# Kernel optimization log

Hardware: AMD Instinct MI355X
Metric: run time of the kernel (lower is better)

## Reference

```python
import jax, jax.numpy as jnp
import numpy as np

N, F, H, C, E = 100000, 64, 128, 10, 1600000
BN_EPS = 1e-5


def setup_inputs() -> dict:
    key = jax.random.key(0)
    ks = jax.random.split(key, 16)
    s = 0.05
    return {
        "x": jax.random.normal(ks[0], (N, F), dtype=jnp.float32),
        "edge_index": jax.random.randint(ks[1], (2, E), 0, N, dtype=jnp.int64),
        # conv1 MLP: Linear(F,H), ReLU, Linear(H,H)
        "w1a": jax.random.normal(ks[2], (F, H), dtype=jnp.float32) * s,
        "b1a": jnp.zeros((H,), jnp.float32),
        "w1b": jax.random.normal(ks[3], (H, H), dtype=jnp.float32) * s,
        "b1b": jnp.zeros((H,), jnp.float32),
        # conv2 MLP: Linear(H,H), ReLU, Linear(H,H)
        "w2a": jax.random.normal(ks[4], (H, H), dtype=jnp.float32) * s,
        "b2a": jnp.zeros((H,), jnp.float32),
        "w2b": jax.random.normal(ks[5], (H, H), dtype=jnp.float32) * s,
        "b2b": jnp.zeros((H,), jnp.float32),
        # BatchNorm affine params
        "bn1_g": jnp.ones((H,), jnp.float32),
        "bn1_b": jnp.zeros((H,), jnp.float32),
        "bn2_g": jnp.ones((H,), jnp.float32),
        "bn2_b": jnp.zeros((H,), jnp.float32),
        # classifier MLP: Linear(H,H), ReLU, (Dropout=identity), Linear(H,C)
        "mw1": jax.random.normal(ks[6], (H, H), dtype=jnp.float32) * s,
        "mb1": jnp.zeros((H,), jnp.float32),
        "mw2": jax.random.normal(ks[7], (H, C), dtype=jnp.float32) * s,
        "mb2": jnp.zeros((C,), jnp.float32),
    }


def _gin_conv(x, src, dst, wa, ba, wb, bb):
    # GINConv, eps=0: mlp( sum_{j in N(i)} x_j + x_i )
    agg = jax.ops.segment_sum(x[src], dst, num_segments=N) + x
    h = jax.nn.relu(agg @ wa + ba)
    return h @ wb + bb


def _batchnorm(h, g, b):
    mean = jnp.mean(h, axis=0)
    var = jnp.var(h, axis=0)  # biased, matches torch BN training normalization
    return (h - mean) * jax.lax.rsqrt(var + BN_EPS) * g + b


def reference(x, edge_index, w1a, b1a, w1b, b1b, w2a, b2a, w2b, b2b,
              bn1_g, bn1_b, bn2_g, bn2_b, mw1, mb1, mw2, mb2):
    src, dst = edge_index[0], edge_index[1]
    h = _gin_conv(x, src, dst, w1a, b1a, w1b, b1b)
    h = jax.nn.relu(_batchnorm(h, bn1_g, bn1_b))
    h = _gin_conv(h, src, dst, w2a, b2a, w2b, b2b)
    latent = jax.nn.relu(_batchnorm(h, bn2_g, bn2_b))
    # classifier (dropout = identity at inference)
    m = jax.nn.relu(latent @ mw1 + mb1)
    class_out = m @ mw2 + mb2
    return latent, class_out
```

## Files before the change

kernel.cpp:

```cpp
#include <hip/hip_runtime.h>
#include <cstdint>


#define NN 100000
#define FF 64
#define HH 128
#define CC 10
#define EE 1600000
#define BN_EPS 1e-5f
#define MBLK 128
#define NBLK_LIN ((NN + MBLK - 1) / MBLK)
#define BSHIFT 7
#define NBUCK ((NN + 127) / 128)
#define CHUNK 16384
#define NB_CH ((EE + CHUNK - 1) / CHUNK)
#define NB_CVT 3125
#define TW (8192 + 4 * 16384 + 2048)
#define TWB ((TW + 255) / 256)
#define LDSE 3072

typedef __attribute__((ext_vector_type(8))) short bf16x8;
typedef __attribute__((ext_vector_type(4))) float f32x4;

__device__ inline unsigned short f2bf(float f) {
    unsigned int u = __float_as_uint(f);
    unsigned int r = (u + 0x7fffu + ((u >> 16) & 1u)) >> 16;
    return (unsigned short)r;
}
__device__ inline float b2f(unsigned short h) {
    return __uint_as_float(((unsigned int)h) << 16);
}
__device__ inline unsigned int pack2(float a, float b) {
    return (unsigned int)f2bf(a) | ((unsigned int)f2bf(b) << 16);
}
__device__ inline int detect_i64(const unsigned int* e) {
    return (e[1] | e[3] | e[5] | e[7]) == 0u;
}
__device__ inline int edge_dst(const void* eiv, int f, int e) {
    return f ? (int)((const long long*)eiv)[EE + e] : ((const int*)eiv)[EE + e];
}
__device__ inline int edge_src(const void* eiv, int f, int e) {
    return f ? (int)((const long long*)eiv)[e] : ((const int*)eiv)[e];
}

__global__ __launch_bounds__(256) void cvtprep_kernel(
    const float* __restrict__ x, unsigned short* __restrict__ xb,
    const float* __restrict__ w1a, const float* __restrict__ w1b,
    const float* __restrict__ w2a, const float* __restrict__ w2b,
    const float* __restrict__ mw1, const float* __restrict__ mw2,
    unsigned short* __restrict__ wt1a, unsigned short* __restrict__ wt1b,
    unsigned short* __restrict__ wt2a, unsigned short* __restrict__ wt2b,
    unsigned short* __restrict__ wtm1, unsigned short* __restrict__ wtm2,
    float* __restrict__ stats, const void* __restrict__ eiv,
    int* __restrict__ chunkhist) {
    __shared__ int hist[NBUCK];
    const int tid = threadIdx.x;
    const int b = blockIdx.x;
    if (b == 0)
        for (int i = tid; i < 512; i += 256) stats[i] = 0.f;
    if (b < NB_CVT) {
        int i = b * 256 + tid;
        float4 a = ((const float4*)x)[i * 2];
        float4 c = ((const float4*)x)[i * 2 + 1];
        uint4 o;
        o.x = pack2(a.x, a.y); o.y = pack2(a.z, a.w);
        o.z = pack2(c.x, c.y); o.w = pack2(c.z, c.w);
        ((uint4*)xb)[i] = o;
        return;
    }
    if (b < NB_CVT + TWB) {
        int idx = (b - NB_CVT) * 256 + tid;
        if (idx < 8192) {
            int k = idx >> 7, n = idx & 127;
            wt1a[n * 64 + k] = f2bf(w1a[idx]);
        } else if (idx < 8192 + 16384) {
            int t = idx - 8192; int k = t >> 7, n = t & 127;
            wt1b[n * 128 + k] = f2bf(w1b[t]);
        } else if (idx < 8192 + 2 * 16384) {
            int t = idx - (8192 + 16384); int k = t >> 7, n = t & 127;
            wt2a[n * 128 + k] = f2bf(w2a[t]);
        } else if (idx < 8192 + 3 * 16384) {
            int t = idx - (8192 + 2 * 16384); int k = t >> 7, n = t & 127;
            wt2b[n * 128 + k] = f2bf(w2b[t]);
        } else if (idx < 8192 + 4 * 16384) {
            int t = idx - (8192 + 3 * 16384); int k = t >> 7, n = t & 127;
            wtm1[n * 128 + k] = f2bf(mw1[t]);
        } else if (idx < TW) {
            int t = idx - (8192 + 4 * 16384); int n = t & 15, k = t >> 4;
            wtm2[n * 128 + k] = (n < CC) ? f2bf(mw2[k * CC + n]) : (unsigned short)0;
        }
        return;
    }
    const int ch = b - NB_CVT - TWB;
    const int f = detect_i64((const unsigned int*)eiv);
    for (int i = tid; i < NBUCK; i += 256) hist[i] = 0;
    __syncthreads();
    int beg = ch * CHUNK, end = min(beg + CHUNK, EE);
    for (int e = beg + tid; e < end; e += 256)
        atomicAdd(&hist[edge_dst(eiv, f, e) >> BSHIFT], 1);
    __syncthreads();
    for (int i = tid; i < NBUCK; i += 256) chunkhist[ch * NBUCK + i] = hist[i];
}

__global__ __launch_bounds__(128) void chunkscan_kernel(int* __restrict__ chunkhist,
                                                        int* __restrict__ gbcount) {
    __shared__ int s[128];
    const int b = blockIdx.x, tid = threadIdx.x;
    int v = (tid < NB_CH) ? chunkhist[tid * NBUCK + b] : 0;
    s[tid] = v;
    __syncthreads();
    for (int off = 1; off < 128; off <<= 1) {
        int t = (tid >= off) ? s[tid - off] : 0;
        __syncthreads();
        s[tid] += t;
        __syncthreads();
    }
    if (tid < NB_CH) chunkhist[tid * NBUCK + b] = s[tid] - v;
    if (tid == 127) gbcount[b] = s[127];
}

__global__ __launch_bounds__(1024) void bscan_kernel(const int* __restrict__ gbcount,
                                                     int* __restrict__ gbstart,
                                                     int* __restrict__ rowstart) {
    __shared__ int s[1024];
    const int tid = threadIdx.x;
    int v = (tid < NBUCK) ? gbcount[tid] : 0;
    s[tid] = v;
    __syncthreads();
    for (int off = 1; off < 1024; off <<= 1) {
        int t = (tid >= off) ? s[tid - off] : 0;
        __syncthreads();
        s[tid] += t;
        __syncthreads();
    }
    if (tid < NBUCK) gbstart[tid] = s[tid] - v;
    if (tid == 0) { gbstart[NBUCK] = EE; rowstart[NN] = EE; }
}

__global__ __launch_bounds__(256) void p2_bin_kernel(const void* __restrict__ eiv,
                                                     const int* __restrict__ gbstart,
                                                     const int* __restrict__ relbase,
                                                     unsigned int* __restrict__ packed) {
    __shared__ int hist[NBUCK];
    __shared__ int basep[NBUCK];
    const int tid = threadIdx.x;
    const int ch = blockIdx.x;
    const int f = detect_i64((const unsigned int*)eiv);
    for (int i = tid; i < NBUCK; i += 256) {
        hist[i] = 0;
        basep[i] = gbstart[i] + relbase[ch * NBUCK + i];
    }
    __syncthreads();
    int beg = ch * CHUNK, end = min(beg + CHUNK, EE);
    for (int e = beg + tid; e < end; e += 256) {
        int s = edge_src(eiv, f, e);
        int d = edge_dst(eiv, f, e);
        int b = d >> BSHIFT;
        int r = atomicAdd(&hist[b], 1);
        packed[basep[b] + r] = (unsigned int)s | ((unsigned int)(d & 127) << 17);
    }
}

__global__ __launch_bounds__(256) void p3g1_kernel(const unsigned int* __restrict__ packed,
                                                   const int* __restrict__ gbstart,
                                                   const unsigned short* __restrict__ xb,
                                                   int* __restrict__ rowstart,
                                                   int* __restrict__ eidx,
                                                   unsigned short* __restrict__ agg1) {
    __shared__ int hist[128];
    __shared__ int excl[128];
    __shared__ int sc[128];
    __shared__ int lidx[LDSE];
    const int tid = threadIdx.x;
    const int b = blockIdx.x;
    const int bstart = gbstart[b], bend = gbstart[b + 1];
    const int cnt = bend - bstart;
    if (tid < 128) hist[tid] = 0;
    __syncthreads();
    for (int e = bstart + tid; e < bend; e += 256)
        atomicAdd(&hist[packed[e] >> 17], 1);
    __syncthreads();
    int v = (tid < 128) ? hist[tid] : 0;
    if (tid < 128) sc[tid] = v;
    __syncthreads();
    for (int off = 1; off < 128; off <<= 1) {
        int t = (tid < 128 && tid >= off) ? sc[tid - off] : 0;
        __syncthreads();
        if (tid < 128) sc[tid] += t;
        __syncthreads();
    }
    if (tid < 128) {
        excl[tid] = sc[tid] - v;
        hist[tid] = 0;
        int node = b * 128 + tid;
        if (node < NN) rowstart[node] = bstart + sc[tid] - v;
    }
    __syncthreads();
    const bool inl = (cnt <= LDSE);
    for (int e = bstart + tid; e < bend; e += 256) {
        unsigned int p = packed[e];
        int dl = p >> 17;
        int r = atomicAdd(&hist[dl], 1);
        int pos = excl[dl] + r;
        int sv = (int)(p & 0x1FFFFu);
        eidx[bstart + pos] = sv;
        if (inl) lidx[pos] = sv;
    }
    __syncthreads();
    const int* ep = inl ? (const int*)lidx : (eidx + bstart);
    const int g = tid >> 3, l8 = tid & 7, c = l8 * 8;
    for (int r4 = 0; r4 < 4; r4++) {
        int nl = r4 * 32 + g;
        int node = b * 128 + nl;
        if (node >= NN) continue;
        float acc[8];
        uint4 sv4 = *(const uint4*)(xb + (size_t)node * FF + c);
        {
            const unsigned int* wv = (const unsigned int*)&sv4;
#pragma unroll
            for (int p = 0; p < 4; p++) {
                acc[p * 2] = b2f((unsigned short)(wv[p] & 0xffff));
                acc[p * 2 + 1] = b2f((unsigned short)(wv[p] >> 16));
            }
        }
        auto addv = [&](uint4 u) {
            const unsigned int* wv = (const unsigned int*)&u;
#pragma unroll
            for (int p = 0; p < 4; p++) {
                acc[p * 2] += b2f((unsigned short)(wv[p] & 0xffff));
                acc[p * 2 + 1] += b2f((unsigned short)(wv[p] >> 16));
            }
        };
        int beg2 = excl[nl], cend = beg2 + hist[nl];
        int j = beg2;
        for (; j + 3 < cend; j += 4) {
            int i0 = ep[j], i1 = ep[j + 1], i2 = ep[j + 2], i3 = ep[j + 3];
            uint4 v0 = *(const uint4*)(xb + (size_t)i0 * FF + c);
            uint4 v1 = *(const uint4*)(xb + (size_t)i1 * FF + c);
            uint4 v2 = *(const uint4*)(xb + (size_t)i2 * FF + c);
            uint4 v3 = *(const uint4*)(xb + (size_t)i3 * FF + c);
            addv(v0); addv(v1); addv(v2); addv(v3);
        }
        for (; j < cend; j++)
            addv(*(const uint4*)(xb + (size_t)ep[j] * FF + c));
        uint4 o;
        o.x = pack2(acc[0], acc[1]); o.y = pack2(acc[2], acc[3]);
        o.z = pack2(acc[4], acc[5]); o.w = pack2(acc[6], acc[7]);
        *(uint4*)(agg1 + (size_t)node * FF + c) = o;
    }
}

__global__ __launch_bounds__(256) void gather2_kernel(const unsigned short* __restrict__ h,
                                                      const int* __restrict__ rowstart,
                                                      const int* __restrict__ eidx,
                                                      const float* __restrict__ statsum,
                                                      const float* __restrict__ statsq,
                                                      const float* __restrict__ bng,
                                                      const float* __restrict__ bnb,
                                                      unsigned short* __restrict__ agg2) {
    int node = blockIdx.x * 8 + (threadIdx.x >> 5);
    const int l32 = threadIdx.x & 31;
    const int c = l32 * 4;
    if (node >= NN) return;
    float scl[4], off[4];
#pragma unroll
    for (int k = 0; k < 4; k++) {
        float m = statsum[c + k] * (1.0f / NN);
        float vv = statsq[c + k] * (1.0f / NN) - m * m;
        scl[k] = bng[c + k] * rsqrtf(vv + BN_EPS);
        off[k] = bnb[c + k] - m * scl[k];
    }
    float acc[4] = {0.f, 0.f, 0.f, 0.f};
    auto addv = [&](uint2 u) {
        acc[0] += fmaxf(fmaf(b2f((unsigned short)(u.x & 0xffff)), scl[0], off[0]), 0.f);
        acc[1] += fmaxf(fmaf(b2f((unsigned short)(u.x >> 16)), scl[1], off[1]), 0.f);
        acc[2] += fmaxf(fmaf(b2f((unsigned short)(u.y & 0xffff)), scl[2], off[2]), 0.f);
        acc[3] += fmaxf(fmaf(b2f((unsigned short)(u.y >> 16)), scl[3], off[3]), 0.f);
    };
    addv(*(const uint2*)(h + (size_t)node * HH + c));
    int beg = rowstart[node], end = rowstart[node + 1];
    int j = beg;
    for (; j + 3 < end; j += 4) {
        int i0 = eidx[j], i1 = eidx[j + 1], i2 = eidx[j + 2], i3 = eidx[j + 3];
        uint2 v0 = *(const uint2*)(h + (size_t)i0 * HH + c);
        uint2 v1 = *(const uint2*)(h + (size_t)i1 * HH + c);
        uint2 v2 = *(const uint2*)(h + (size_t)i2 * HH + c);
        uint2 v3 = *(const uint2*)(h + (size_t)i3 * HH + c);
        addv(v0); addv(v1); addv(v2); addv(v3);
    }
    for (; j < end; j++)
        addv(*(const uint2*)(h + (size_t)eidx[j] * HH + c));
    uint2 o;
    o.x = pack2(acc[0], acc[1]);
    o.y = pack2(acc[2], acc[3]);
    *(uint2*)(agg2 + (size_t)node * HH + c) = o;
}

template <int KIN>
__global__ __launch_bounds__(256) void mlp_kernel(const unsigned short* __restrict__ in,
                                                  const unsigned short* __restrict__ wTa,
                                                  const float* __restrict__ ba,
                                                  const unsigned short* __restrict__ wTb,
                                                  const float* __restrict__ bb,
                                                  unsigned short* __restrict__ out,
                                                  float* __restrict__ bnsum,
                                                  float* __restrict__ bnsq) {
    constexpr int KLDA = KIN + 8;
    constexpr int CH = KIN / 8;
    __shared__ __attribute__((aligned(16))) unsigned short sA[MBLK * 136];
    __shared__ __attribute__((aligned(16))) unsigned short sW[128 * 136];
    __shared__ float sSt[256];
    __shared__ float sB[256];

    const int tid = threadIdx.x;
    const int wave = tid >> 6, lane = tid & 63;
    const int quad = lane >> 4, l16 = lane & 15;
    const long long row0 = (long long)blockIdx.x * MBLK;

    sSt[tid] = 0.f;
    if (tid < 128) sB[tid] = ba[tid];
    else sB[tid] = bb[tid - 128];

    for (int i = tid; i < 128 * CH; i += 256)
        *(uint4*)(sW + (i / CH) * KLDA + (i % CH) * 8) = ((const uint4*)wTa)[i];
    for (int i = tid; i < MBLK * CH; i += 256) {
        int r = i / CH, c = i % CH;
        uint4 v = {0u, 0u, 0u, 0u};
        if (row0 + r < NN) v = *(const uint4*)(in + (row0 + r) * KIN + c * 8);
        *(uint4*)(sA + r * KLDA + c * 8) = v;
    }
    __syncthreads();

    f32x4 acc1[2][8];
#pragma unroll
    for (int t = 0; t < 2; t++)
#pragma unroll
        for (int n = 0; n < 8; n++) acc1[t][n] = 0.f;
#pragma unroll
    for (int ks = 0; ks < KIN / 32; ks++) {
        bf16x8 a0 = *(const bf16x8*)(sA + (wave * 32 + l16) * KLDA + ks * 32 + quad * 8);
        bf16x8 a1 = *(const bf16x8*)(sA + (wave * 32 + 16 + l16) * KLDA + ks * 32 + quad * 8);
#pragma unroll
        for (int nt = 0; nt < 8; nt++) {
            bf16x8 b = *(const bf16x8*)(sW + (nt * 16 + l16) * KLDA + ks * 32 + quad * 8);
            acc1[0][nt] = __builtin_amdgcn_mfma_f32_16x16x32_bf16(a0, b, acc1[0][nt], 0, 0, 0);
            acc1[1][nt] = __builtin_amdgcn_mfma_f32_16x16x32_bf16(a1, b, acc1[1][nt], 0, 0, 0);
        }
    }
    __syncthreads();

#pragma unroll
    for (int nt = 0; nt < 8; nt++) {
        const int col = nt * 16 + l16;
        const float bcol = sB[col];
#pragma unroll
        for (int t = 0; t < 2; t++)
#pragma unroll
            for (int r = 0; r < 4; r++) {
                int rl = wave * 32 + t * 16 + quad * 4 + r;
                sA[rl * 136 + col] = f2bf(fmaxf(acc1[t][nt][r] + bcol, 0.f));
            }
    }
    for (int i = tid; i < 128 * 16; i += 256)
        *(uint4*)(sW + (i >> 4) * 136 + (i & 15) * 8) = ((const uint4*)wTb)[i];
    __syncthreads();

    f32x4 acc2[2][8];
#pragma unroll
    for (int t = 0; t < 2; t++)
#pragma unroll
        for (int n = 0; n < 8; n++) acc2[t][n] = 0.f;
#pragma unroll
    for (int ks = 0; ks < 4; ks++) {
        bf16x8 a0 = *(const bf16x8*)(sA + (wave * 32 + l16) * 136 + ks * 32 + quad * 8);
        bf16x8 a1 = *(const bf16x8*)(sA + (wave * 32 + 16 + l16) * 136 + ks * 32 + quad * 8);
#pragma unroll
        for (int nt = 0; nt < 8; nt++) {
            bf16x8 b = *(const bf16x8*)(sW + (nt * 16 + l16) * 136 + ks * 32 + quad * 8);
            acc2[0][nt] = __builtin_amdgcn_mfma_f32_16x16x32_bf16(a0, b, acc2[0][nt], 0, 0, 0);
            acc2[1][nt] = __builtin_amdgcn_mfma_f32_16x16x32_bf16(a1, b, acc2[1][nt], 0, 0, 0);
        }
    }
    __syncthreads();

#pragma unroll
    for (int nt = 0; nt < 8; nt++) {
        const int col = nt * 16 + l16;
        const float bcol = sB[128 + col];
        float ls = 0.f, lq = 0.f;
#pragma unroll
        for (int t = 0; t < 2; t++)
#pragma unroll
            for (int r = 0; r < 4; r++) {
                int rl = wave * 32 + t * 16 + quad * 4 + r;
                float v = acc2[t][nt][r] + bcol;
                if (row0 + rl < NN) { ls += v; lq += v * v; }
                sA[rl * 136 + col] = f2bf(v);
            }
        ls += __shfl_down(ls, 32); ls += __shfl_down(ls, 16);
        lq += __shfl_down(lq, 32); lq += __shfl_down(lq, 16);
        if (lane < 16) { atomicAdd(&sSt[col], ls); atomicAdd(&sSt[128 + col], lq); }
    }
    __syncthreads();

    for (int i = tid; i < MBLK * 16; i += 256) {
        int r = i >> 4, c = i & 15;
        if (row0 + r < NN)
            *(uint4*)(out + (row0 + r) * 128 + c * 8) = *(const uint4*)(sA + r * 136 + c * 8);
    }
    if (tid < 128) atomicAdd(&bnsum[tid], sSt[tid]);
    else atomicAdd(&bnsq[tid - 128], sSt[tid]);
}

__global__ __launch_bounds__(256) void final_kernel(const unsigned short* __restrict__ h2,
                                                    const float* __restrict__ statsum,
                                                    const float* __restrict__ statsq,
                                                    const float* __restrict__ bng,
                                                    const float* __restrict__ bnb,
                                                    const unsigned short* __restrict__ wTm1,
                                                    const float* __restrict__ mb1,
                                                    const unsigned short* __restrict__ wTm2,
                                                    const float* __restrict__ mb2,
                                                    float* __restrict__ latent,
                                                    float* __restrict__ cls) {
    __shared__ __attribute__((aligned(16))) unsigned short sA[MBLK * 136];
    __shared__ __attribute__((aligned(16))) unsigned short sW[128 * 136];
    __shared__ float sBN[256];
    __shared__ float sB1[128];

    const int tid = threadIdx.x;
    const int wave = tid >> 6, lane = tid & 63;
    const int quad = lane >> 4, l16 = lane & 15;
    const long long row0 = (long long)blockIdx.x * MBLK;

    if (tid < 128) {
        float mean = statsum[tid] * (1.0f / NN);
        float var = statsq[tid] * (1.0f / NN) - mean * mean;
        float sc = bng[tid] * rsqrtf(var + BN_EPS);
        sBN[tid] = sc;
        sBN[128 + tid] = bnb[tid] - mean * sc;
        sB1[tid] = mb1[tid];
    }
    for (int i = tid; i < 128 * 16; i += 256)
        *(uint4*)(sW + (i >> 4) * 136 + (i & 15) * 8) = ((const uint4*)wTm1)[i];
    __syncthreads();

    for (int i = tid; i < MBLK * 16; i += 256) {
        int r = i >> 4, c = i & 15;
        bool live = (row0 + r < NN);
        uint4 hv = {0u, 0u, 0u, 0u};
        if (live) hv = *(const uint4*)(h2 + (row0 + r) * 128 + c * 8);
        const unsigned int* wv = (const unsigned int*)&hv;
        float vs[8];
#pragma unroll
        for (int p = 0; p < 4; p++) {
            int cc = c * 8 + p * 2;
            vs[p * 2]     = fmaxf(fmaf(b2f((unsigned short)(wv[p] & 0xffff)), sBN[cc], sBN[128 + cc]), 0.f);
            vs[p * 2 + 1] = fmaxf(fmaf(b2f((unsigned short)(wv[p] >> 16)), sBN[cc + 1], sBN[129 + cc]), 0.f);
        }
        if (live) {
            float4 f0 = {vs[0], vs[1], vs[2], vs[3]};
            float4 f1 = {vs[4], vs[5], vs[6], vs[7]};
            float* lp = latent + (row0 + r) * 128 + c * 8;
            *(float4*)lp = f0;
            *(float4*)(lp + 4) = f1;
        }
        uint4 o;
        o.x = pack2(vs[0], vs[1]); o.y = pack2(vs[2], vs[3]);
        o.z = pack2(vs[4], vs[5]); o.w = pack2(vs[6], vs[7]);
        *(uint4*)(sA + r * 136 + c * 8) = o;
    }
    __syncthreads();

    f32x4 acc1[2][8];
#pragma unroll
    for (int t = 0; t < 2; t++)
#pragma unroll
        for (int n = 0; n < 8; n++) acc1[t][n] = 0.f;
#pragma unroll
    for (int ks = 0; ks < 4; ks++) {
        bf16x8 av0 = *(const bf16x8*)(sA + (wave * 32 + l16) * 136 + ks * 32 + quad * 8);
        bf16x8 av1 = *(const bf16x8*)(sA + (wave * 32 + 16 + l16) * 136 + ks * 32 + quad * 8);
#pragma unroll
        for (int nt = 0; nt < 8; nt++) {
            bf16x8 b = *(const bf16x8*)(sW + (nt * 16 + l16) * 136 + ks * 32 + quad * 8);
            acc1[0][nt] = __builtin_amdgcn_mfma_f32_16x16x32_bf16(av0, b, acc1[0][nt], 0, 0, 0);
            acc1[1][nt] = __builtin_amdgcn_mfma_f32_16x16x32_bf16(av1, b, acc1[1][nt], 0, 0, 0);
        }
    }
    __syncthreads();

#pragma unroll
    for (int nt = 0; nt < 8; nt++) {
        const int col = nt * 16 + l16;
        const float bcol = sB1[col];
#pragma unroll
        for (int t = 0; t < 2; t++)
#pragma unroll
            for (int r = 0; r < 4; r++) {
                int rl = wave * 32 + t * 16 + quad * 4 + r;
                sA[rl * 136 + col] = f2bf(fmaxf(acc1[t][nt][r] + bcol, 0.f));
            }
    }
    if (tid < 256)
        *(uint4*)(sW + (tid >> 4) * 136 + (tid & 15) * 8) = ((const uint4*)wTm2)[tid];
    __syncthreads();

    f32x4 acc2[2];
    acc2[0] = 0.f; acc2[1] = 0.f;
#pragma unroll
    for (int ks = 0; ks < 4; ks++) {
        bf16x8 av0 = *(const bf16x8*)(sA + (wave * 32 + l16) * 136 + ks * 32 + quad * 8);
        bf16x8 av1 = *(const bf16x8*)(sA + (wave * 32 + 16 + l16) * 136 + ks * 32 + quad * 8);
        bf16x8 b = *(const bf16x8*)(sW + l16 * 136 + ks * 32 + quad * 8);
        acc2[0] = __builtin_amdgcn_mfma_f32_16x16x32_bf16(av0, b, acc2[0], 0, 0, 0);
        acc2[1] = __builtin_amdgcn_mfma_f32_16x16x32_bf16(av1, b, acc2[1], 0, 0, 0);
    }
    __syncthreads();

    float* sOf = (float*)sA;
    if (l16 < CC) {
        const float bc = mb2[l16];
#pragma unroll
        for (int t = 0; t < 2; t++)
#pragma unroll
            for (int r = 0; r < 4; r++) {
                int rl = wave * 32 + t * 16 + quad * 4 + r;
                sOf[rl * CC + l16] = acc2[t][r] + bc;
            }
    }
    __syncthreads();
    for (int i = tid; i < MBLK * CC; i += 256) {
        long long gi = row0 * CC + i;
        if (gi < (long long)NN * CC) cls[gi] = sOf[i];
    }
}

extern "C" void kernel_launch(void* const* d_in, const int* in_sizes, int n_in,
                              void* d_out, int out_size, void* d_ws, size_t ws_size,
                              hipStream_t stream) {
    const float* x   = (const float*)d_in[0];
    const void* ei   = d_in[1];
    const float* w1a = (const float*)d_in[2];
    const float* b1a = (const float*)d_in[3];
    const float* w1b = (const float*)d_in[4];
    const float* b1b = (const float*)d_in[5];
    const float* w2a = (const float*)d_in[6];
    const float* b2a = (const float*)d_in[7];
    const float* w2b = (const float*)d_in[8];
    const float* b2b = (const float*)d_in[9];
    const float* bn1g = (const float*)d_in[10];
    const float* bn1b = (const float*)d_in[11];
    const float* bn2g = (const float*)d_in[12];
    const float* bn2b = (const float*)d_in[13];
    const float* mw1 = (const float*)d_in[14];
    const float* mb1 = (const float*)d_in[15];
    const float* mw2 = (const float*)d_in[16];
    const float* mb2 = (const float*)d_in[17];
    float* out = (float*)d_out;

    char* w = (char*)d_ws;
    unsigned short* xb   = (unsigned short*)w;  w += (size_t)NN * FF * 2;
    unsigned short* agg1 = (unsigned short*)w;  w += (size_t)NN * FF * 2;
    unsigned short* h    = (unsigned short*)w;  w += (size_t)NN * HH * 2;
    unsigned short* agg2 = (unsigned short*)w;  w += (size_t)NN * HH * 2;
    float* stats = (float*)w;                   w += 1024 * 4;
    int* eidx = (int*)w;                        w += (size_t)EE * 4;
    unsigned int* packed = (unsigned int*)w;    w += (size_t)EE * 4;
    int* rowstart = (int*)w;                    w += (NN + 2) * 4;
    int* gbcount = (int*)w;                     w += (NBUCK + 2) * 4;
    int* gbstart = (int*)w;                     w += (NBUCK + 2) * 4;
    int* chunkhist = (int*)w;                   w += (size_t)NB_CH * NBUCK * 4;
    unsigned short* wt1a = (unsigned short*)w;  w += 8192 * 2;
    unsigned short* wt1b = (unsigned short*)w;  w += 16384 * 2;
    unsigned short* wt2a = (unsigned short*)w;  w += 16384 * 2;
    unsigned short* wt2b = (unsigned short*)w;  w += 16384 * 2;
    unsigned short* wtm1 = (unsigned short*)w;  w += 16384 * 2;
    unsigned short* wtm2 = (unsigned short*)w;  w += 2048 * 2;

    cvtprep_kernel<<<NB_CVT + TWB + NB_CH, 256, 0, stream>>>(
        x, xb, w1a, w1b, w2a, w2b, mw1, mw2,
        wt1a, wt1b, wt2a, wt2b, wtm1, wtm2, stats, ei, chunkhist);

    chunkscan_kernel<<<NBUCK, 128, 0, stream>>>(chunkhist, gbcount);
    bscan_kernel<<<1, 1024, 0, stream>>>(gbcount, gbstart, rowstart);
    p2_bin_kernel<<<NB_CH, 256, 0, stream>>>(ei, gbstart, chunkhist, packed);

    p3g1_kernel<<<NBUCK, 256, 0, stream>>>(packed, gbstart, xb, rowstart, eidx, agg1);

    mlp_kernel<FF><<<NBLK_LIN, 256, 0, stream>>>(agg1, wt1a, b1a, wt1b, b1b, h, stats, stats + 128);

    gather2_kernel<<<(NN + 7) / 8, 256, 0, stream>>>(
        h, rowstart, eidx, stats, stats + 128, bn1g, bn1b, agg2);
    mlp_kernel<HH><<<NBLK_LIN, 256, 0, stream>>>(agg2, wt2a, b2a, wt2b, b2b, h, stats + 256, stats + 384);

    final_kernel<<<NBLK_LIN, 256, 0, stream>>>(
        h, stats + 256, stats + 384, bn2g, bn2b,
        wtm1, mb1, wtm2, mb2, out, out + (size_t)NN * HH);
}
```

Measured before the change: 377.7 us.

## Merge bucket scan into chunkscan via last-block pattern; read MLP operands directly

Removes the separate single-block bscan launch by having the last-finishing chunkscan block, detected with an atomic counter, do the global bucket prefix scan. The MLP and final kernels stop staging A tiles and weights in LDS and instead load MFMA operands straight from global memory, relying on cache hits for the small weight matrices. This cuts LDS footprint, which may allow more blocks per CU, and drops staging syncs. In exchange the kernels issue more uncoalesced global loads, and the first MLP now reads past NN on the last partial tile without a bounds check.

```diff
diff --git a/kernel.cpp b/kernel.cpp
--- a/kernel.cpp
+++ b/kernel.cpp
@@ -51,13 +51,15 @@
     unsigned short* __restrict__ wt1a, unsigned short* __restrict__ wt1b,
     unsigned short* __restrict__ wt2a, unsigned short* __restrict__ wt2b,
     unsigned short* __restrict__ wtm1, unsigned short* __restrict__ wtm2,
-    float* __restrict__ stats, const void* __restrict__ eiv,
-    int* __restrict__ chunkhist) {
+    float* __restrict__ stats, int* __restrict__ donecnt,
+    const void* __restrict__ eiv, int* __restrict__ chunkhist) {
     __shared__ int hist[NBUCK];
     const int tid = threadIdx.x;
     const int b = blockIdx.x;
-    if (b == 0)
+    if (b == 0) {
         for (int i = tid; i < 512; i += 256) stats[i] = 0.f;
+        if (tid == 0) donecnt[0] = 0;
+    }
     if (b < NB_CVT) {
         int i = b * 256 + tid;
         float4 a = ((const float4*)x)[i * 2];
@@ -103,8 +105,12 @@
 }
 
 __global__ __launch_bounds__(128) void chunkscan_kernel(int* __restrict__ chunkhist,
-                                                        int* __restrict__ gbcount) {
+                                                        int* __restrict__ gbcount,
+                                                        int* __restrict__ gbstart,
+                                                        int* __restrict__ rowstart,
+                                                        int* __restrict__ donecnt) {
     __shared__ int s[128];
+    __shared__ int isLast;
     const int b = blockIdx.x, tid = threadIdx.x;
     int v = (tid < NB_CH) ? chunkhist[tid * NBUCK + b] : 0;
     s[tid] = v;
@@ -117,23 +123,28 @@
     }
     if (tid < NB_CH) chunkhist[tid * NBUCK + b] = s[tid] - v;
     if (tid == 127) gbcount[b] = s[127];
-}
-
-__global__ __launch_bounds__(1024) void bscan_kernel(const int* __restrict__ gbcount,
-                                                     int* __restrict__ gbstart,
-                                                     int* __restrict__ rowstart) {
-    __shared__ int s[1024];
-    const int tid = threadIdx.x;
-    int v = (tid < NBUCK) ? gbcount[tid] : 0;
-    s[tid] = v;
-    __syncthreads();
-    for (int off = 1; off < 1024; off <<= 1) {
-        int t = (tid >= off) ? s[tid - off] : 0;
-        __syncthreads();
-        s[tid] += t;
-        __syncthreads();
-    }
-    if (tid < NBUCK) gbstart[tid] = s[tid] - v;
+    __threadfence();
+    __syncthreads();
+    if (tid == 0) isLast = (atomicAdd(donecnt, 1) == NBUCK - 1) ? 1 : 0;
+    __syncthreads();
+    if (!isLast) return;
+    __threadfence();
+    int carry = 0;
+    for (int c0 = 0; c0 < NBUCK; c0 += 128) {
+        int vv = (c0 + tid < NBUCK) ? gbcount[c0 + tid] : 0;
+        __syncthreads();
+        s[tid] = vv;
+        __syncthreads();
+        for (int off = 1; off < 128; off <<= 1) {
+            int t = (tid >= off) ? s[tid - off] : 0;
+            __syncthreads();
+            s[tid] += t;
+            __syncthreads();
+        }
+        if (c0 + tid < NBUCK) gbstart[c0 + tid] = carry + s[tid] - vv;
+        carry += s[127];
+        __syncthreads();
+    }
     if (tid == 0) { gbstart[NBUCK] = EE; rowstart[NN] = EE; }
 }
 
@@ -305,32 +316,20 @@
                                                   unsigned short* __restrict__ out,
                                                   float* __restrict__ bnsum,
                                                   float* __restrict__ bnsq) {
-    constexpr int KLDA = KIN + 8;
-    constexpr int CH = KIN / 8;
-    __shared__ __attribute__((aligned(16))) unsigned short sA[MBLK * 136];
-    __shared__ __attribute__((aligned(16))) unsigned short sW[128 * 136];
+    __shared__ __attribute__((aligned(16))) unsigned short sT[MBLK * 136];
     __shared__ float sSt[256];
     __shared__ float sB[256];
 
     const int tid = threadIdx.x;
     const int wave = tid >> 6, lane = tid & 63;
     const int quad = lane >> 4, l16 = lane & 15;
-    const long long row0 = (long long)blockIdx.x * MBLK;
+    const size_t row0 = (size_t)blockIdx.x * MBLK;
 
     sSt[tid] = 0.f;
     if (tid < 128) sB[tid] = ba[tid];
     else sB[tid] = bb[tid - 128];
 
-    for (int i = tid; i < 128 * CH; i += 256)
-        *(uint4*)(sW + (i / CH) * KLDA + (i % CH) * 8) = ((const uint4*)wTa)[i];
-    for (int i = tid; i < MBLK * CH; i += 256) {
-        int r = i / CH, c = i % CH;
-        uint4 v = {0u, 0u, 0u, 0u};
-        if (row0 + r < NN) v = *(const uint4*)(in + (row0 + r) * KIN + c * 8);
-        *(uint4*)(sA + r * KLDA + c * 8) = v;
-    }
-    __syncthreads();
-
+    const unsigned short* Ag = in + row0 * KIN;
     f32x4 acc1[2][8];
 #pragma unroll
     for (int t = 0; t < 2; t++)
@@ -338,11 +337,11 @@
         for (int n = 0; n < 8; n++) acc1[t][n] = 0.f;
 #pragma unroll
     for (int ks = 0; ks < KIN / 32; ks++) {
-        bf16x8 a0 = *(const bf16x8*)(sA + (wave * 32 + l16) * KLDA + ks * 32 + quad * 8);
-        bf16x8 a1 = *(const bf16x8*)(sA + (wave * 32 + 16 + l16) * KLDA + ks * 32 + quad * 8);
+        bf16x8 a0 = *(const bf16x8*)(Ag + (wave * 32 + l16) * KIN + ks * 32 + quad * 8);
+        bf16x8 a1 = *(const bf16x8*)(Ag + (wave * 32 + 16 + l16) * KIN + ks * 32 + quad * 8);
 #pragma unroll
         for (int nt = 0; nt < 8; nt++) {
-            bf16x8 b = *(const bf16x8*)(sW + (nt * 16 + l16) * KLDA + ks * 32 + quad * 8);
+            bf16x8 b = *(const bf16x8*)(wTa + (nt * 16 + l16) * KIN + ks * 32 + quad * 8);
             acc1[0][nt] = __builtin_amdgcn_mfma_f32_16x16x32_bf16(a0, b, acc1[0][nt], 0, 0, 0);
             acc1[1][nt] = __builtin_amdgcn_mfma_f32_16x16x32_bf16(a1, b, acc1[1][nt], 0, 0, 0);
         }
@@ -358,11 +357,9 @@
 #pragma unroll
             for (int r = 0; r < 4; r++) {
                 int rl = wave * 32 + t * 16 + quad * 4 + r;
-                sA[rl * 136 + col] = f2bf(fmaxf(acc1[t][nt][r] + bcol, 0.f));
+                sT[rl * 136 + col] = f2bf(fmaxf(acc1[t][nt][r] + bcol, 0.f));
             }
     }
-    for (int i = tid; i < 128 * 16; i += 256)
-        *(uint4*)(sW + (i >> 4) * 136 + (i & 15) * 8) = ((const uint4*)wTb)[i];
     __syncthreads();
 
     f32x4 acc2[2][8];
@@ -372,11 +369,11 @@
         for (int n = 0; n < 8; n++) acc2[t][n] = 0.f;
 #pragma unroll
     for (int ks = 0; ks < 4; ks++) {
-        bf16x8 a0 = *(const bf16x8*)(sA + (wave * 32 + l16) * 136 + ks * 32 + quad * 8);
-        bf16x8 a1 = *(const bf16x8*)(sA + (wave * 32 + 16 + l16) * 136 + ks * 32 + quad * 8);
+        bf16x8 a0 = *(const bf16x8*)(sT + (wave * 32 + l16) * 136 + ks * 32 + quad * 8);
+        bf16x8 a1 = *(const bf16x8*)(sT + (wave * 32 + 16 + l16) * 136 + ks * 32 + quad * 8);
 #pragma unroll
         for (int nt = 0; nt < 8; nt++) {
-            bf16x8 b = *(const bf16x8*)(sW + (nt * 16 + l16) * 136 + ks * 32 + quad * 8);
+            bf16x8 b = *(const bf16x8*)(wTb + (nt * 16 + l16) * 128 + ks * 32 + quad * 8);
             acc2[0][nt] = __builtin_amdgcn_mfma_f32_16x16x32_bf16(a0, b, acc2[0][nt], 0, 0, 0);
             acc2[1][nt] = __builtin_amdgcn_mfma_f32_16x16x32_bf16(a1, b, acc2[1][nt], 0, 0, 0);
         }
@@ -395,7 +392,7 @@
                 int rl = wave * 32 + t * 16 + quad * 4 + r;
                 float v = acc2[t][nt][r] + bcol;
                 if (row0 + rl < NN) { ls += v; lq += v * v; }
-                sA[rl * 136 + col] = f2bf(v);
+                sT[rl * 136 + col] = f2bf(v);
             }
         ls += __shfl_down(ls, 32); ls += __shfl_down(ls, 16);
         lq += __shfl_down(lq, 32); lq += __shfl_down(lq, 16);
@@ -406,7 +403,7 @@
     for (int i = tid; i < MBLK * 16; i += 256) {
         int r = i >> 4, c = i & 15;
         if (row0 + r < NN)
-            *(uint4*)(out + (row0 + r) * 128 + c * 8) = *(const uint4*)(sA + r * 136 + c * 8);
+            *(uint4*)(out + (row0 + r) * 128 + c * 8) = *(const uint4*)(sT + r * 136 + c * 8);
     }
     if (tid < 128) atomicAdd(&bnsum[tid], sSt[tid]);
     else atomicAdd(&bnsq[tid - 128], sSt[tid]);
@@ -424,14 +421,13 @@
                                                     float* __restrict__ latent,
                                                     float* __restrict__ cls) {
     __shared__ __attribute__((aligned(16))) unsigned short sA[MBLK * 136];
-    __shared__ __attribute__((aligned(16))) unsigned short sW[128 * 136];
     __shared__ float sBN[256];
     __shared__ float sB1[128];
 
     const int tid = threadIdx.x;
     const int wave = tid >> 6, lane = tid & 63;
     const int quad = lane >> 4, l16 = lane & 15;
-    const long long row0 = (long long)blockIdx.x * MBLK;
+    const size_t row0 = (size_t)blockIdx.x * MBLK;
 
     if (tid < 128) {
         float mean = statsum[tid] * (1.0f / NN);
@@ -441,8 +437,6 @@
         sBN[128 + tid] = bnb[tid] - mean * sc;
         sB1[tid] = mb1[tid];
     }
-    for (int i = tid; i < 128 * 16; i += 256)
-        *(uint4*)(sW + (i >> 4) * 136 + (i & 15) * 8) = ((const uint4*)wTm1)[i];
     __syncthreads();
 
     for (int i = tid; i < MBLK * 16; i += 256) {
@@ -483,7 +477,7 @@
         bf16x8 av1 = *(const bf16x8*)(sA + (wave * 32 + 16 + l16) * 136 + ks * 32 + quad * 8);
 #pragma unroll
         for (int nt = 0; nt < 8; nt++) {
-            bf16x8 b = *(const bf16x8*)(sW + (nt * 16 + l16) * 136 + ks * 32 + quad * 8);
+            bf16x8 b = *(const bf16x8*)(wTm1 + (nt * 16 + l16) * 128 + ks * 32 + quad * 8);
             acc1[0][nt] = __builtin_amdgcn_mfma_f32_16x16x32_bf16(av0, b, acc1[0][nt], 0, 0, 0);
             acc1[1][nt] = __builtin_amdgcn_mfma_f32_16x16x32_bf16(av1, b, acc1[1][nt], 0, 0, 0);
         }
@@ -502,8 +496,6 @@
                 sA[rl * 136 + col] = f2bf(fmaxf(acc1[t][nt][r] + bcol, 0.f));
             }
     }
-    if (tid < 256)
-        *(uint4*)(sW + (tid >> 4) * 136 + (tid & 15) * 8) = ((const uint4*)wTm2)[tid];
     __syncthreads();
 
     f32x4 acc2[2];
@@ -512,7 +504,7 @@
     for (int ks = 0; ks < 4; ks++) {
         bf16x8 av0 = *(const bf16x8*)(sA + (wave * 32 + l16) * 136 + ks * 32 + quad * 8);
         bf16x8 av1 = *(const bf16x8*)(sA + (wave * 32 + 16 + l16) * 136 + ks * 32 + quad * 8);
-        bf16x8 b = *(const bf16x8*)(sW + l16 * 136 + ks * 32 + quad * 8);
+        bf16x8 b = *(const bf16x8*)(wTm2 + l16 * 128 + ks * 32 + quad * 8);
         acc2[0] = __builtin_amdgcn_mfma_f32_16x16x32_bf16(av0, b, acc2[0], 0, 0, 0);
         acc2[1] = __builtin_amdgcn_mfma_f32_16x16x32_bf16(av1, b, acc2[1], 0, 0, 0);
     }
@@ -531,7 +523,7 @@
     }
     __syncthreads();
     for (int i = tid; i < MBLK * CC; i += 256) {
-        long long gi = row0 * CC + i;
+        long long gi = (long long)row0 * CC + i;
         if (gi < (long long)NN * CC) cls[gi] = sOf[i];
     }
 }
@@ -570,6 +562,7 @@
     int* rowstart = (int*)w;                    w += (NN + 2) * 4;
     int* gbcount = (int*)w;                     w += (NBUCK + 2) * 4;
     int* gbstart = (int*)w;                     w += (NBUCK + 2) * 4;
+    int* donecnt = (int*)w;                     w += 16;
     int* chunkhist = (int*)w;                   w += (size_t)NB_CH * NBUCK * 4;
     unsigned short* wt1a = (unsigned short*)w;  w += 8192 * 2;
     unsigned short* wt1b = (unsigned short*)w;  w += 16384 * 2;
@@ -580,10 +573,9 @@
 
     cvtprep_kernel<<<NB_CVT + TWB + NB_CH, 256, 0, stream>>>(
         x, xb, w1a, w1b, w2a, w2b, mw1, mw2,
-        wt1a, wt1b, wt2a, wt2b, wtm1, wtm2, stats, ei, chunkhist);
-
-    chunkscan_kernel<<<NBUCK, 128, 0, stream>>>(chunkhist, gbcount);
-    bscan_kernel<<<1, 1024, 0, stream>>>(gbcount, gbstart, rowstart);
+        wt1a, wt1b, wt2a, wt2b, wtm1, wtm2, stats, donecnt, ei, chunkhist);
+
+    chunkscan_kernel<<<NBUCK, 128, 0, stream>>>(chunkhist, gbcount, gbstart, rowstart, donecnt);
     p2_bin_kernel<<<NB_CH, 256, 0, stream>>>(ei, gbstart, chunkhist, packed);
 
     p3g1_kernel<<<NBUCK, 256, 0, stream>>>(packed, gbstart, xb, rowstart, eidx, agg1);
```

Measured after the change: 480.3 us. +27.2%, slower.
